# Optimization experiments

Hardware: AMD Instinct MI355X
Metric: run time of the kernel (lower is better)

The kernel has to match this reference:

```python
import jax, jax.numpy as jnp
import numpy as np

N, T, C = 8, 2048, 1024   # batch, seq_len, n_embd (== num_cls)
NUM_CLS = 1024
LID, TL = 6, 12


def setup_inputs() -> dict:
    key = jax.random.key(0)
    ks = jax.random.split(key, 5)
    s = 1.0 / np.sqrt(C)
    x = jax.random.normal(ks[0], (N, T, C), jnp.float32)
    Wk = jax.random.normal(ks[1], (C, C), jnp.float32) * s
    Wv = jax.random.normal(ks[2], (C, C), jnp.float32) * s
    Wr = jax.random.normal(ks[3], (C, C), jnp.float32) * s
    Wo = jax.random.normal(ks[4], (NUM_CLS, C), jnp.float32) * s
    # faithful time-parameter initialization from __init__
    r0 = LID / (TL - 1)            # ratio_0_to_1
    r1 = 1.0 - LID / TL            # ratio_1_to_almost0
    ddd = (np.arange(C, dtype=np.float32) / C).reshape(1, 1, C)
    time_mix_k = jnp.asarray(ddd ** r1)
    time_mix_v = jnp.asarray(ddd ** r1 + 0.3 * r0)
    time_mix_r = jnp.asarray(ddd ** (0.5 * r1))
    time_decay = jnp.zeros((C,), jnp.float32)                 # decay_speed init
    time_first = jnp.full((C,), np.log(0.3), jnp.float32)
    last_x = jnp.zeros((N, 1, C), jnp.float32)                # init_x repeated
    state = jnp.zeros((N, 3, 1, C), jnp.float32)              # init_state repeated
    return {"x": x, "it": 0, "Wk": Wk, "Wv": Wv, "Wr": Wr, "Wo": Wo,
            "time_mix_k": time_mix_k, "time_mix_v": time_mix_v,
            "time_mix_r": time_mix_r, "time_decay": time_decay,
            "time_first": time_first, "last_x": last_x, "state": state}


def _wkv_with_eps(w, u, k, v, state):
    """Numerically-stabilized RWKV wkv scan. k,v: (N,T,C); state: (N,3,1,C)."""
    alpha = state[:, 0, -1]  # (N,C)
    beta = state[:, 1, -1]
    eps = state[:, 2, -1]

    def step(carry, kv):
        a, b, e = carry
        kt, vt = kv                      # each (N,C)
        ukt = u + kt
        tau = jnp.maximum(ukt, e)
        e1 = jnp.exp(e - tau)
        e2 = jnp.exp(ukt - tau)
        wkv_t = (e1 * a + e2 * vt) / (e1 * b + e2)
        w_eps = e - w
        e_n = jnp.maximum(w_eps, kt)
        e1n = jnp.exp(w_eps - e_n)
        e2n = jnp.exp(kt - e_n)
        return (e1n * a + e2n * vt, e1n * b + e2n, e_n), wkv_t

    kT = jnp.swapaxes(k, 0, 1)  # (T,N,C)
    vT = jnp.swapaxes(v, 0, 1)
    (alpha, beta, eps), wkv = jax.lax.scan(step, (alpha, beta, eps), (kT, vT))
    wkv = jnp.swapaxes(wkv, 0, 1)  # (N,T,C)
    last_state = jnp.stack([alpha, beta, eps], axis=1)[:, :, None, :]  # (N,3,1,C)
    return wkv, last_state


def reference(x, it, Wk, Wv, Wr, Wo, time_mix_k, time_mix_v, time_mix_r,
              time_decay, time_first, last_x, state):
    # time-mix blend (last_x = init_x zeros, broadcast over T as in the source)
    k = (x * time_mix_k + last_x * (1.0 - time_mix_k)) @ Wk.T
    v = (x * time_mix_v + last_x * (1.0 - time_mix_v)) @ Wv.T
    r = (x * time_mix_r + last_x * (1.0 - time_mix_r)) @ Wr.T
    sr = jax.nn.sigmoid(r)
    w = jnp.exp(time_decay)
    u = time_first
    wkv, _last_state = _wkv_with_eps(w, u, k, v, state)
    rwkv = (wkv * sr) @ Wo.T  # (N,T,NUM_CLS)
    return rwkv
```

## Files before the change

### kernel.cpp

```cpp
#include <hip/hip_runtime.h>
#include <hip/hip_bf16.h>
#include <stdint.h>


typedef float f4 __attribute__((ext_vector_type(4)));
typedef short bh8 __attribute__((ext_vector_type(8)));
typedef unsigned int u32;
typedef unsigned short u16;

__device__ __forceinline__ u32 cvt2bf(float a, float b) {
    __hip_bfloat162 h = __float22bfloat162_rn(make_float2(a, b));
    u32 u; __builtin_memcpy(&u, &h, 4); return u;
}
__device__ __forceinline__ float b2f(u16 u) {
    u32 x = (u32)u << 16; float f; __builtin_memcpy(&f, &x, 4); return f;
}
__device__ __forceinline__ u16 f2b(float f) {
    __hip_bfloat16 h = __float2bfloat16(f);
    u16 u; __builtin_memcpy(&u, &h, 2); return u;
}
__device__ __forceinline__ void gld_lds16(const void* g, void* l) {
    __builtin_amdgcn_global_load_lds(
        (const __attribute__((address_space(1))) u32*)g,
        (__attribute__((address_space(3))) u32*)l, 16, 0, 0);
}


#define BAR() __builtin_amdgcn_s_barrier()

#define PH_MFMA(I0, J0) \
  BAR(); \
  asm volatile("s_waitcnt lgkmcnt(0)" ::: "memory"); \
  __builtin_amdgcn_s_setprio(1); \
  _Pragma("unroll") for (int ks = 0; ks < 2; ks++) \
  _Pragma("unroll") for (int i = 0; i < 4; i++) \
  _Pragma("unroll") for (int j = 0; j < 2; j++) \
    acc[(I0)+i][(J0)+j] = __builtin_amdgcn_mfma_f32_16x16x32_bf16( \
        af[i][ks], bf[(J0)+j][ks], acc[(I0)+i][(J0)+j], 0, 0, 0); \
  __builtin_amdgcn_s_setprio(0);

#define GBODY(cA, cB, nA, nB, KKN, STG) do { \
  const u16* ap0 = (cA) + (wm + fr) * 64 + cs0; \
  const u16* ap1 = (cA) + (wm + fr) * 64 + (cs0 ^ 32); \
  const u16* bp0 = (cB) + (wn + fr) * 64 + cs0; \
  const u16* bp1 = (cB) + (wn + fr) * 64 + (cs0 ^ 32); \
  bh8 af[4][2], bf[4][2]; \
   \
  _Pragma("unroll") for (int i = 0; i < 4; i++) { \
    af[i][0] = *(const bh8*)(ap0 + i * 1024); af[i][1] = *(const bh8*)(ap1 + i * 1024); } \
  _Pragma("unroll") for (int j = 0; j < 2; j++) { \
    bf[j][0] = *(const bh8*)(bp0 + j * 1024); bf[j][1] = *(const bh8*)(bp1 + j * 1024); } \
  if (STG) { \
    gld_lds16(gB + srcB_lane + (KKN),                 (nB) + w * 1024); \
    gld_lds16(gB + srcB_lane + 8192 + (KKN),          (nB) + w * 1024 + 512); \
    gld_lds16(gB + srcB_lane + 131072 + (KKN),        (nB) + 8192 + w * 1024); \
    gld_lds16(gB + srcB_lane + 131072 + 8192 + (KKN), (nB) + 8192 + w * 1024 + 512); } \
  PH_MFMA(0, 0); \
  BAR(); \
   \
  _Pragma("unroll") for (int j = 0; j < 2; j++) { \
    bf[2 + j][0] = *(const bh8*)(bp0 + (2 + j) * 1024); bf[2 + j][1] = *(const bh8*)(bp1 + (2 + j) * 1024); } \
  if (STG) { \
    gld_lds16(gA + srcA_lane + (KKN),          (nA) + w * 512); \
    gld_lds16(gA + srcA_lane + 131072 + (KKN), (nA) + 8192 + w * 512); } \
  PH_MFMA(0, 2); \
  if (STG) { asm volatile("s_waitcnt vmcnt(6)" ::: "memory"); } \
  else     { asm volatile("s_waitcnt vmcnt(0)" ::: "memory"); } \
  BAR(); \
   \
  _Pragma("unroll") for (int i = 0; i < 4; i++) { \
    af[i][0] = *(const bh8*)(ap0 + (4 + i) * 1024); af[i][1] = *(const bh8*)(ap1 + (4 + i) * 1024); } \
  if (STG) gld_lds16(gA + srcA_lane + 65536 + (KKN), (nA) + 4096 + w * 512); \
  PH_MFMA(4, 0); \
  BAR(); \
   \
  if (STG) gld_lds16(gA + srcA_lane + 131072 + 65536 + (KKN), (nA) + 12288 + w * 512); \
  PH_MFMA(4, 2); \
  if (STG) { asm volatile("s_waitcnt vmcnt(2)" ::: "memory"); } \
  BAR(); \
} while (0)

template<int EPI>
__global__ __launch_bounds__(512, 2) void gemm256(
    const u16* __restrict__ Ag, const u16* __restrict__ Bg, const float* __restrict__ bias,
    u16* __restrict__ Kb, u16* __restrict__ Vb, u16* __restrict__ SRb, float* __restrict__ Yf)
{
    __shared__ __align__(16) char pool[131072];
    u16* A0s = (u16*)pool;
    u16* B0s = A0s + 16384;
    u16* A1s = B0s + 16384;
    u16* B1s = A1s + 16384;

    const int bid = blockIdx.x;
    const int xcd = bid & 7;
    const int s   = bid >> 3;
    int p, mt, nt;
    if (EPI == 0) { p = s >> 5; int r = s & 31; nt = r & 3; mt = xcd * 8 + (r >> 2); }
    else          { p = 0;                      nt = s & 3; mt = xcd * 8 + (s >> 2); }
    const int n0 = nt * 256;
    const int m0 = mt * 256;

    const u16* gA = Ag + (size_t)m0 * 1024;
    const u16* gB = Bg + (EPI == 0 ? (size_t)p * 1048576 : 0) + (size_t)n0 * 1024;

    const int tid  = threadIdx.x;
    const int w    = tid >> 6;
    const int lane = tid & 63;
    const int wr = w >> 2, wc = w & 3;
    const int wm = wr * 128, wn = wc * 64;
    const int fr = lane & 15, quad = lane >> 4;
    const int cs0 = (quad ^ (fr & 7)) * 8;

    const int l8 = lane >> 3, l7 = lane & 7;
    const int chs = (l7 ^ l8) * 8;
    const int srcA_lane = (w * 8 + l8) * 1024 + chs;
    const int srcB_lane = (w * 16 + l8) * 1024 + chs;

    f4 acc[8][4];
#pragma unroll
    for (int i = 0; i < 8; i++)
#pragma unroll
        for (int j = 0; j < 4; j++) { f4 z = {0.f, 0.f, 0.f, 0.f}; acc[i][j] = z; }

#pragma unroll
    for (int q = 0; q < 4; q++)
        gld_lds16(gA + srcA_lane + q * 65536, A0s + q * 4096 + w * 512);
#pragma unroll
    for (int H = 0; H < 2; H++)
#pragma unroll
        for (int c = 0; c < 2; c++)
            gld_lds16(gB + srcB_lane + H * 131072 + c * 8192, B0s + H * 8192 + w * 1024 + c * 512);
    asm volatile("s_waitcnt vmcnt(0)" ::: "memory");
    BAR();

    for (int t = 0; t < 14; t += 2) {
        GBODY(A0s, B0s, A1s, B1s, (t + 1) * 64, true);
        GBODY(A1s, B1s, A0s, B0s, (t + 2) * 64, true);
    }
    GBODY(A0s, B0s, A1s, B1s, 15 * 64, true);
    GBODY(A1s, B1s, A0s, B0s, 0, false);

    if constexpr (EPI == 0) {
        const int batch = m0 >> 11;
        float bv[4];
#pragma unroll
        for (int j = 0; j < 4; j++) bv[j] = bias[p * 8192 + batch * 1024 + n0 + wn + j * 16 + fr];
        __syncthreads();
        u16* S = (u16*)pool;
#pragma unroll
        for (int i = 0; i < 8; i++)
#pragma unroll
            for (int j = 0; j < 4; j++)
#pragma unroll
                for (int r = 0; r < 4; r++) {
                    float v = acc[i][j][r] + bv[j];
                    if (p == 2) v = __fdividef(1.0f, 1.0f + __expf(-v));
                    int row = wm + i * 16 + quad * 4 + r;
                    int col = wn + j * 16 + fr;
                    int phys = (col >> 3) ^ (quad << 3);
                    S[row * 256 + phys * 8 + (col & 7)] = f2b(v);
                }
        __syncthreads();
        u16* Y = p == 0 ? Kb : (p == 1 ? Vb : SRb);
#pragma unroll
        for (int rep = 0; rep < 16; rep++) {
            int cid = rep * 512 + tid;
            int row = cid >> 5, ch = cid & 31;
            int phys = ch ^ (((row >> 2) & 3) << 3);
            uint4 val = *(const uint4*)(S + row * 256 + phys * 8);
            *(uint4*)(Y + (size_t)(m0 + row) * 1024 + n0 + ch * 8) = val;
        }
    } else {
        float* Sf = (float*)pool;
#pragma unroll
        for (int h = 0; h < 2; h++) {
            __syncthreads();
            if (wr == h) {
#pragma unroll
                for (int i = 0; i < 8; i++)
#pragma unroll
                    for (int j = 0; j < 4; j++)
#pragma unroll
                        for (int r = 0; r < 4; r++) {
                            int row = i * 16 + quad * 4 + r;
                            int col = wn + j * 16 + fr;
                            int phys = (col >> 2) ^ (quad << 4);
                            Sf[row * 256 + phys * 4 + (col & 3)] = acc[i][j][r];
                        }
            }
            __syncthreads();
#pragma unroll
            for (int rep = 0; rep < 16; rep++) {
                int cid = rep * 512 + tid;
                int row = cid >> 6, ch = cid & 63;
                int phys = ch ^ (((row >> 2) & 3) << 4);
                f4 val = *(const f4*)(Sf + row * 256 + phys * 4);
                *(f4*)(Yf + (size_t)(m0 + h * 128 + row) * 1024 + n0 + ch * 4) = val;
            }
        }
    }
}

__global__ __launch_bounds__(256) void prep_all(
    const float* __restrict__ x, const float* __restrict__ lastx,
    const float* __restrict__ Wk, const float* __restrict__ Wv,
    const float* __restrict__ Wr, const float* __restrict__ Wo,
    const float* __restrict__ tmk, const float* __restrict__ tmv, const float* __restrict__ tmr,
    u16* __restrict__ xb, u16* __restrict__ Wall, float* __restrict__ bias)
{
    int b = blockIdx.x;
    if (b < 16384) {
        int e = (b * 256 + threadIdx.x) << 2;
        f4 v = *(const f4*)(x + e);
        *(uint2*)(xb + e) = make_uint2(cvt2bf(v.x, v.y), cvt2bf(v.z, v.w));
    } else if (b < 20480) {
        int e = ((b - 16384) * 256 + threadIdx.x) << 2;
        int wid = e >> 20;
        int off = e & 1048575;
        int c = e & 1023;
        const float* src = wid == 0 ? Wk : (wid == 1 ? Wv : (wid == 2 ? Wr : Wo));
        f4 v = *(const f4*)(src + off);
        if (wid < 3) {
            const float* m = wid == 0 ? tmk : (wid == 1 ? tmv : tmr);
            v = v * *(const f4*)(m + c);
        }
        *(uint2*)(Wall + e) = make_uint2(cvt2bf(v.x, v.y), cvt2bf(v.z, v.w));
    } else {
        int wid = (b - 20480) * 4 + (threadIdx.x >> 6);
        int lane = threadIdx.x & 63;
        int proj = wid >> 10;
        int n = wid & 1023;
        const float* W = proj == 0 ? Wk : (proj == 1 ? Wv : Wr);
        const float* m = proj == 0 ? tmk : (proj == 1 ? tmv : tmr);
        float acc[8];
#pragma unroll
        for (int bb = 0; bb < 8; bb++) acc[bb] = 0.f;
        for (int c = lane; c < 1024; c += 64) {
            float wc = W[n * 1024 + c] * (1.0f - m[c]);
#pragma unroll
            for (int bb = 0; bb < 8; bb++) acc[bb] = fmaf(lastx[bb * 1024 + c], wc, acc[bb]);
        }
#pragma unroll
        for (int bb = 0; bb < 8; bb++) {
            float v = acc[bb];
#pragma unroll
            for (int sh = 32; sh >= 1; sh >>= 1) v += __shfl_xor(v, sh);
            if (lane == 0) bias[proj * 8192 + bb * 1024 + n] = v;
        }
    }
}

__global__ __launch_bounds__(256) void wkv_pass1(
    const u16* __restrict__ Kp, const u16* __restrict__ Vp,
    const float* __restrict__ tdec,
    float* __restrict__ Ca, float* __restrict__ Cb, float* __restrict__ Ce)
{
    int tid = blockIdx.x * 256 + threadIdx.x;
    int c = (tid & 511) << 1;
    int chunk = (tid >> 9) & 63;
    int n = tid >> 15;
    float w0 = __expf(tdec[c]), w1 = __expf(tdec[c + 1]);
    int base = (n * 2048 + chunk * 32) * 1024 + c;
    float a0 = 0.f, b0 = 0.f, e0 = -1e30f;
    float a1 = 0.f, b1 = 0.f, e1 = -1e30f;
#pragma unroll 4
    for (int i = 0; i < 32; i++) {
        u32 ku = *(const u32*)(Kp + base + (i << 10));
        u32 vu = *(const u32*)(Vp + base + (i << 10));
        float k0 = b2f((u16)ku), k1 = b2f((u16)(ku >> 16));
        float v0 = b2f((u16)vu), v1 = b2f((u16)(vu >> 16));
        float en0 = fmaxf(e0 - w0, k0);
        float f10 = __expf(e0 - w0 - en0), f20 = __expf(k0 - en0);
        a0 = fmaf(f10, a0, f20 * v0); b0 = fmaf(f10, b0, f20); e0 = en0;
        float en1 = fmaxf(e1 - w1, k1);
        float f11 = __expf(e1 - w1 - en1), f21 = __expf(k1 - en1);
        a1 = fmaf(f11, a1, f21 * v1); b1 = fmaf(f11, b1, f21); e1 = en1;
    }
    int oidx = ((n * 64 + chunk) << 10) + c;
    *(float2*)(Ca + oidx) = make_float2(a0, a1);
    *(float2*)(Cb + oidx) = make_float2(b0, b1);
    *(float2*)(Ce + oidx) = make_float2(e0, e1);
}

__global__ __launch_bounds__(256) void wkv_pass2(
    const float* __restrict__ state, const float* __restrict__ tdec,
    float* Ca, float* Cb, float* Ce)
{
    int tid = blockIdx.x * 256 + threadIdx.x;
    int c = tid & 1023;
    int n = tid >> 10;
    float a = state[(n * 3 + 0) * 1024 + c];
    float b = state[(n * 3 + 1) * 1024 + c];
    float e = state[(n * 3 + 2) * 1024 + c];
    float wL = __expf(tdec[c]) * 32.0f;
    for (int ch = 0; ch < 64; ++ch) {
        int idx = ((n * 64 + ch) << 10) + c;
        float ca = Ca[idx], cb = Cb[idx], ce = Ce[idx];
        Ca[idx] = a; Cb[idx] = b; Ce[idx] = e;
        float en = fmaxf(e - wL, ce);
        float f1 = __expf(e - wL - en);
        float f2 = __expf(ce - en);
        a = fmaf(f1, a, f2 * ca);
        b = fmaf(f1, b, f2 * cb);
        e = en;
    }
}

__global__ __launch_bounds__(256) void wkv_pass3(
    const u16* __restrict__ Kp, const u16* __restrict__ Vp, const u16* __restrict__ SRp,
    const float* __restrict__ Sa, const float* __restrict__ Sb, const float* __restrict__ Se,
    const float* __restrict__ tfirst, const float* __restrict__ tdec,
    u16* __restrict__ Pp)
{
    int tid = blockIdx.x * 256 + threadIdx.x;
    int c = (tid & 511) << 1;
    int chunk = (tid >> 9) & 63;
    int n = tid >> 15;
    int sidx = ((n * 64 + chunk) << 10) + c;
    float a0 = Sa[sidx], b0 = Sb[sidx], e0 = Se[sidx];
    float a1 = Sa[sidx + 1], b1 = Sb[sidx + 1], e1 = Se[sidx + 1];
    float u0 = tfirst[c], u1 = tfirst[c + 1];
    float w0 = __expf(tdec[c]), w1 = __expf(tdec[c + 1]);
    int base = (n * 2048 + chunk * 32) * 1024 + c;
#pragma unroll 2
    for (int i = 0; i < 32; i++) {
        u32 ku = *(const u32*)(Kp + base + (i << 10));
        u32 vu = *(const u32*)(Vp + base + (i << 10));
        u32 su = *(const u32*)(SRp + base + (i << 10));
        float k0 = b2f((u16)ku), k1 = b2f((u16)(ku >> 16));
        float v0 = b2f((u16)vu), v1 = b2f((u16)(vu >> 16));
        float s0 = b2f((u16)su), s1 = b2f((u16)(su >> 16));
        float t0 = fmaxf(u0 + k0, e0);
        float x10 = __expf(e0 - t0), x20 = __expf(u0 + k0 - t0);
        float wkv0 = __fdividef(fmaf(x10, a0, x20 * v0), fmaf(x10, b0, x20));
        float t1 = fmaxf(u1 + k1, e1);
        float x11 = __expf(e1 - t1), x21 = __expf(u1 + k1 - t1);
        float wkv1 = __fdividef(fmaf(x11, a1, x21 * v1), fmaf(x11, b1, x21));
        *(u32*)(Pp + base + (i << 10)) = (u32)f2b(wkv0 * s0) | ((u32)f2b(wkv1 * s1) << 16);
        float en0 = fmaxf(e0 - w0, k0);
        float f10 = __expf(e0 - w0 - en0), f20 = __expf(k0 - en0);
        a0 = fmaf(f10, a0, f20 * v0); b0 = fmaf(f10, b0, f20); e0 = en0;
        float en1 = fmaxf(e1 - w1, k1);
        float f11 = __expf(e1 - w1 - en1), f21 = __expf(k1 - en1);
        a1 = fmaf(f11, a1, f21 * v1); b1 = fmaf(f11, b1, f21); e1 = en1;
    }
}

extern "C" void kernel_launch(void* const* d_in, const int* in_sizes, int n_in,
                              void* d_out, int out_size, void* d_ws, size_t ws_size,
                              hipStream_t stream) {
    const float* x      = (const float*)d_in[0];
    const float* Wk     = (const float*)d_in[2];
    const float* Wv     = (const float*)d_in[3];
    const float* Wr     = (const float*)d_in[4];
    const float* Wo     = (const float*)d_in[5];
    const float* tmk    = (const float*)d_in[6];
    const float* tmv    = (const float*)d_in[7];
    const float* tmr    = (const float*)d_in[8];
    const float* tdec   = (const float*)d_in[9];
    const float* tfirst = (const float*)d_in[10];
    const float* lastx  = (const float*)d_in[11];
    const float* state  = (const float*)d_in[12];
    float* out = (float*)d_out;

    const size_t MB = 1024ull * 1024ull;
    char* ws = (char*)d_ws;
    u16* Kb   = (u16*)(ws);
    u16* Vb   = (u16*)(ws + 32 * MB);
    u16* SRb  = (u16*)(ws + 64 * MB);
    u16* xb   = (u16*)(ws + 96 * MB);
    u16* Wall = (u16*)(ws + 128 * MB);
    float* bias = (float*)(ws + 136 * MB);
    float* Ca = (float*)(ws + 137 * MB);
    float* Cb = (float*)(ws + 139 * MB);
    float* Ce = (float*)(ws + 141 * MB);
    u16* Pb = xb;

    dim3 blk(256);
    prep_all<<<21248, blk, 0, stream>>>(x, lastx, Wk, Wv, Wr, Wo, tmk, tmv, tmr, xb, Wall, bias);
    gemm256<0><<<dim3(768), dim3(512), 0, stream>>>(xb, Wall, bias, Kb, Vb, SRb, nullptr);
    wkv_pass1<<<1024, blk, 0, stream>>>(Kb, Vb, tdec, Ca, Cb, Ce);
    wkv_pass2<<<32, blk, 0, stream>>>(state, tdec, Ca, Cb, Ce);
    wkv_pass3<<<1024, blk, 0, stream>>>(Kb, Vb, SRb, Ca, Cb, Ce, tfirst, tdec, Pb);
    gemm256<1><<<dim3(256), dim3(512), 0, stream>>>(Pb, Wall + 3145728, nullptr,
                                                    nullptr, nullptr, nullptr, out);
}
```

Baseline: 358.7 us.

## Replace 256x256 GEMM with 256x128 tile, BK=32, triple-buffered LDS pipeline

Both GEMMs move from a 512-thread 256x256 tile with BK=64 double buffering to a 256-thread 256x128 tile with BK=32 and three LDS stages. The grid doubles and LDS drops from 128KB to 72KB, which should allow more blocks per CU and better load balance across the 256 CUs. Global loads are issued two stages ahead. The epilogues are rewritten to use padded LDS staging in place of XOR swizzles. The trade-off is lower arithmetic intensity per tile (more A reloads) and more barriers per unit of work.

```diff
diff --git a/kernel.cpp b/kernel.cpp
--- a/kernel.cpp
+++ b/kernel.cpp
@@ -25,79 +25,54 @@
         (__attribute__((address_space(3))) u32*)l, 16, 0, 0);
 }
 
-
 #define BAR() __builtin_amdgcn_s_barrier()
 
-#define PH_MFMA(I0, J0) \
+
+#define PH16(I0) \
   BAR(); \
   asm volatile("s_waitcnt lgkmcnt(0)" ::: "memory"); \
   __builtin_amdgcn_s_setprio(1); \
-  _Pragma("unroll") for (int ks = 0; ks < 2; ks++) \
   _Pragma("unroll") for (int i = 0; i < 4; i++) \
-  _Pragma("unroll") for (int j = 0; j < 2; j++) \
-    acc[(I0)+i][(J0)+j] = __builtin_amdgcn_mfma_f32_16x16x32_bf16( \
-        af[i][ks], bf[(J0)+j][ks], acc[(I0)+i][(J0)+j], 0, 0, 0); \
+  _Pragma("unroll") for (int j = 0; j < 4; j++) \
+    acc[(I0)+i][j] = __builtin_amdgcn_mfma_f32_16x16x32_bf16( \
+        af[i], bf[j], acc[(I0)+i][j], 0, 0, 0); \
   __builtin_amdgcn_s_setprio(0);
 
-#define GBODY(cA, cB, nA, nB, KKN, STG) do { \
-  const u16* ap0 = (cA) + (wm + fr) * 64 + cs0; \
-  const u16* ap1 = (cA) + (wm + fr) * 64 + (cs0 ^ 32); \
-  const u16* bp0 = (cB) + (wn + fr) * 64 + cs0; \
-  const u16* bp1 = (cB) + (wn + fr) * 64 + (cs0 ^ 32); \
-  bh8 af[4][2], bf[4][2]; \
-   \
-  _Pragma("unroll") for (int i = 0; i < 4; i++) { \
-    af[i][0] = *(const bh8*)(ap0 + i * 1024); af[i][1] = *(const bh8*)(ap1 + i * 1024); } \
-  _Pragma("unroll") for (int j = 0; j < 2; j++) { \
-    bf[j][0] = *(const bh8*)(bp0 + j * 1024); bf[j][1] = *(const bh8*)(bp1 + j * 1024); } \
+#define GB(CA, CB, NA, NB, KKN, STG, VM) do { \
+  bh8 af[4], bf[4]; \
+  _Pragma("unroll") for (int i = 0; i < 4; i++) af[i] = *(const bh8*)((CA) + apo + i * 512); \
+  _Pragma("unroll") for (int j = 0; j < 4; j++) bf[j] = *(const bh8*)((CB) + bpo + j * 512); \
   if (STG) { \
-    gld_lds16(gB + srcB_lane + (KKN),                 (nB) + w * 1024); \
-    gld_lds16(gB + srcB_lane + 8192 + (KKN),          (nB) + w * 1024 + 512); \
-    gld_lds16(gB + srcB_lane + 131072 + (KKN),        (nB) + 8192 + w * 1024); \
-    gld_lds16(gB + srcB_lane + 131072 + 8192 + (KKN), (nB) + 8192 + w * 1024 + 512); } \
-  PH_MFMA(0, 0); \
+    _Pragma("unroll") for (int q = 0; q < 4; q++) \
+      gld_lds16(gA + sAoff + q * 65536 + (KKN), (NA) + q * 2048 + w * 512); \
+    _Pragma("unroll") for (int h = 0; h < 2; h++) \
+      gld_lds16(gB + sAoff + h * 65536 + (KKN), (NB) + h * 2048 + w * 512); \
+  } \
+  PH16(0); \
   BAR(); \
-   \
-  _Pragma("unroll") for (int j = 0; j < 2; j++) { \
-    bf[2 + j][0] = *(const bh8*)(bp0 + (2 + j) * 1024); bf[2 + j][1] = *(const bh8*)(bp1 + (2 + j) * 1024); } \
-  if (STG) { \
-    gld_lds16(gA + srcA_lane + (KKN),          (nA) + w * 512); \
-    gld_lds16(gA + srcA_lane + 131072 + (KKN), (nA) + 8192 + w * 512); } \
-  PH_MFMA(0, 2); \
-  if (STG) { asm volatile("s_waitcnt vmcnt(6)" ::: "memory"); } \
-  else     { asm volatile("s_waitcnt vmcnt(0)" ::: "memory"); } \
-  BAR(); \
-   \
-  _Pragma("unroll") for (int i = 0; i < 4; i++) { \
-    af[i][0] = *(const bh8*)(ap0 + (4 + i) * 1024); af[i][1] = *(const bh8*)(ap1 + (4 + i) * 1024); } \
-  if (STG) gld_lds16(gA + srcA_lane + 65536 + (KKN), (nA) + 4096 + w * 512); \
-  PH_MFMA(4, 0); \
-  BAR(); \
-   \
-  if (STG) gld_lds16(gA + srcA_lane + 131072 + 65536 + (KKN), (nA) + 12288 + w * 512); \
-  PH_MFMA(4, 2); \
-  if (STG) { asm volatile("s_waitcnt vmcnt(2)" ::: "memory"); } \
+  _Pragma("unroll") for (int i = 0; i < 4; i++) af[i] = *(const bh8*)((CA) + apo + (4 + i) * 512); \
+  PH16(4); \
+  asm volatile("s_waitcnt vmcnt(" VM ")" ::: "memory"); \
   BAR(); \
 } while (0)
 
 template<int EPI>
-__global__ __launch_bounds__(512, 2) void gemm256(
+__global__ __launch_bounds__(256, 2) void gemm_ts(
     const u16* __restrict__ Ag, const u16* __restrict__ Bg, const float* __restrict__ bias,
     u16* __restrict__ Kb, u16* __restrict__ Vb, u16* __restrict__ SRb, float* __restrict__ Yf)
 {
-    __shared__ __align__(16) char pool[131072];
-    u16* A0s = (u16*)pool;
-    u16* B0s = A0s + 16384;
-    u16* A1s = B0s + 16384;
-    u16* B1s = A1s + 16384;
+    __shared__ __align__(16) char pool[73728];
+    u16* A0 = (u16*)pool;          u16* B0 = A0 + 8192;
+    u16* A1 = (u16*)(pool + 24576); u16* B1 = A1 + 8192;
+    u16* A2 = (u16*)(pool + 49152); u16* B2 = A2 + 8192;
 
     const int bid = blockIdx.x;
     const int xcd = bid & 7;
     const int s   = bid >> 3;
     int p, mt, nt;
-    if (EPI == 0) { p = s >> 5; int r = s & 31; nt = r & 3; mt = xcd * 8 + (r >> 2); }
-    else          { p = 0;                      nt = s & 3; mt = xcd * 8 + (s >> 2); }
-    const int n0 = nt * 256;
+    if (EPI == 0) { p = s >> 6; int r = s & 63; nt = r & 7; mt = xcd * 8 + (r >> 3); }
+    else          { p = 0;                      nt = s & 7; mt = xcd * 8 + (s >> 3); }
+    const int n0 = nt * 128;
     const int m0 = mt * 256;
 
     const u16* gA = Ag + (size_t)m0 * 1024;
@@ -106,15 +81,14 @@
     const int tid  = threadIdx.x;
     const int w    = tid >> 6;
     const int lane = tid & 63;
-    const int wr = w >> 2, wc = w & 3;
-    const int wm = wr * 128, wn = wc * 64;
+    const int wm = (w >> 1) * 128, wn = (w & 1) * 64;
     const int fr = lane & 15, quad = lane >> 4;
-    const int cs0 = (quad ^ (fr & 7)) * 8;
-
-    const int l8 = lane >> 3, l7 = lane & 7;
-    const int chs = (l7 ^ l8) * 8;
-    const int srcA_lane = (w * 8 + l8) * 1024 + chs;
-    const int srcB_lane = (w * 16 + l8) * 1024 + chs;
+    const int cs  = (quad ^ ((fr ^ (fr >> 2)) & 3)) * 8;
+    const int apo = (wm + fr) * 32 + cs;
+    const int bpo = (wn + fr) * 32 + cs;
+
+    const int sAoff = (w * 16 + (lane >> 2)) * 1024 +
+                      (((lane & 3) ^ ((lane >> 2) & 3) ^ ((lane >> 4) & 3))) * 8;
 
     f4 acc[8][4];
 #pragma unroll
@@ -123,81 +97,83 @@
         for (int j = 0; j < 4; j++) { f4 z = {0.f, 0.f, 0.f, 0.f}; acc[i][j] = z; }
 
 #pragma unroll
-    for (int q = 0; q < 4; q++)
-        gld_lds16(gA + srcA_lane + q * 65536, A0s + q * 4096 + w * 512);
-#pragma unroll
-    for (int H = 0; H < 2; H++)
-#pragma unroll
-        for (int c = 0; c < 2; c++)
-            gld_lds16(gB + srcB_lane + H * 131072 + c * 8192, B0s + H * 8192 + w * 1024 + c * 512);
-    asm volatile("s_waitcnt vmcnt(0)" ::: "memory");
+    for (int q = 0; q < 4; q++) gld_lds16(gA + sAoff + q * 65536, A0 + q * 2048 + w * 512);
+#pragma unroll
+    for (int h = 0; h < 2; h++) gld_lds16(gB + sAoff + h * 65536, B0 + h * 2048 + w * 512);
+#pragma unroll
+    for (int q = 0; q < 4; q++) gld_lds16(gA + sAoff + q * 65536 + 32, A1 + q * 2048 + w * 512);
+#pragma unroll
+    for (int h = 0; h < 2; h++) gld_lds16(gB + sAoff + h * 65536 + 32, B1 + h * 2048 + w * 512);
+    asm volatile("s_waitcnt vmcnt(6)" ::: "memory");
     BAR();
 
-    for (int t = 0; t < 14; t += 2) {
-        GBODY(A0s, B0s, A1s, B1s, (t + 1) * 64, true);
-        GBODY(A1s, B1s, A0s, B0s, (t + 2) * 64, true);
-    }
-    GBODY(A0s, B0s, A1s, B1s, 15 * 64, true);
-    GBODY(A1s, B1s, A0s, B0s, 0, false);
+    for (int t = 0; t < 30; t += 3) {
+        GB(A0, B0, A2, B2, (t + 2) * 32, 1, "6");
+        GB(A1, B1, A0, B0, (t + 3) * 32, 1, "6");
+        GB(A2, B2, A1, B1, (t + 4) * 32, 1, "6");
+    }
+    GB(A0, B0, A2, B2, 0, 0, "0");
+    GB(A1, B1, A2, B2, 0, 0, "0");
 
     if constexpr (EPI == 0) {
         const int batch = m0 >> 11;
         float bv[4];
 #pragma unroll
         for (int j = 0; j < 4; j++) bv[j] = bias[p * 8192 + batch * 1024 + n0 + wn + j * 16 + fr];
-        __syncthreads();
         u16* S = (u16*)pool;
-#pragma unroll
-        for (int i = 0; i < 8; i++)
-#pragma unroll
-            for (int j = 0; j < 4; j++)
-#pragma unroll
-                for (int r = 0; r < 4; r++) {
-                    float v = acc[i][j][r] + bv[j];
-                    if (p == 2) v = __fdividef(1.0f, 1.0f + __expf(-v));
-                    int row = wm + i * 16 + quad * 4 + r;
-                    int col = wn + j * 16 + fr;
-                    int phys = (col >> 3) ^ (quad << 3);
-                    S[row * 256 + phys * 8 + (col & 7)] = f2b(v);
-                }
-        __syncthreads();
         u16* Y = p == 0 ? Kb : (p == 1 ? Vb : SRb);
 #pragma unroll
-        for (int rep = 0; rep < 16; rep++) {
-            int cid = rep * 512 + tid;
-            int row = cid >> 5, ch = cid & 31;
-            int phys = ch ^ (((row >> 2) & 3) << 3);
-            uint4 val = *(const uint4*)(S + row * 256 + phys * 8);
-            *(uint4*)(Y + (size_t)(m0 + row) * 1024 + n0 + ch * 8) = val;
+        for (int h = 0; h < 2; h++) {
+            __syncthreads();
+            if ((w >> 1) == h) {
+#pragma unroll
+                for (int i = 0; i < 8; i++)
+#pragma unroll
+                    for (int j = 0; j < 4; j++)
+#pragma unroll
+                        for (int r = 0; r < 4; r++) {
+                            float v = acc[i][j][r] + bv[j];
+                            if (p == 2) v = __fdividef(1.0f, 1.0f + __expf(-v));
+                            int row = i * 16 + quad * 4 + r;
+                            int col = wn + j * 16 + fr;
+                            S[row * 136 + col] = f2b(v);
+                        }
+            }
+            __syncthreads();
+#pragma unroll
+            for (int rep = 0; rep < 8; rep++) {
+                int row = rep * 16 + (tid >> 4), ch = tid & 15;
+                uint4 val = *(const uint4*)(S + row * 136 + ch * 8);
+                *(uint4*)(Y + (size_t)(m0 + h * 128 + row) * 1024 + n0 + ch * 8) = val;
+            }
         }
     } else {
         float* Sf = (float*)pool;
 #pragma unroll
-        for (int h = 0; h < 2; h++) {
-            __syncthreads();
-            if (wr == h) {
-#pragma unroll
-                for (int i = 0; i < 8; i++)
-#pragma unroll
-                    for (int j = 0; j < 4; j++)
-#pragma unroll
-                        for (int r = 0; r < 4; r++) {
-                            int row = i * 16 + quad * 4 + r;
-                            int col = wn + j * 16 + fr;
-                            int phys = (col >> 2) ^ (quad << 4);
-                            Sf[row * 256 + phys * 4 + (col & 3)] = acc[i][j][r];
-                        }
+        for (int h = 0; h < 2; h++)
+#pragma unroll
+            for (int ih = 0; ih < 2; ih++) {
+                __syncthreads();
+                if ((w >> 1) == h) {
+#pragma unroll
+                    for (int ii = 0; ii < 4; ii++)
+#pragma unroll
+                        for (int j = 0; j < 4; j++)
+#pragma unroll
+                            for (int r = 0; r < 4; r++) {
+                                int row = ii * 16 + quad * 4 + r;
+                                int col = wn + j * 16 + fr;
+                                Sf[row * 132 + col] = acc[ih * 4 + ii][j][r];
+                            }
+                }
+                __syncthreads();
+#pragma unroll
+                for (int rep = 0; rep < 8; rep++) {
+                    int row = rep * 8 + (tid >> 5), ch = tid & 31;
+                    f4 val = *(const f4*)(Sf + row * 132 + ch * 4);
+                    *(f4*)(Yf + (size_t)(m0 + h * 128 + ih * 64 + row) * 1024 + n0 + ch * 4) = val;
+                }
             }
-            __syncthreads();
-#pragma unroll
-            for (int rep = 0; rep < 16; rep++) {
-                int cid = rep * 512 + tid;
-                int row = cid >> 6, ch = cid & 63;
-                int phys = ch ^ (((row >> 2) & 3) << 4);
-                f4 val = *(const f4*)(Sf + row * 256 + phys * 4);
-                *(f4*)(Yf + (size_t)(m0 + h * 128 + row) * 1024 + n0 + ch * 4) = val;
-            }
-        }
     }
 }
 
@@ -378,10 +354,10 @@
 
     dim3 blk(256);
     prep_all<<<21248, blk, 0, stream>>>(x, lastx, Wk, Wv, Wr, Wo, tmk, tmv, tmr, xb, Wall, bias);
-    gemm256<0><<<dim3(768), dim3(512), 0, stream>>>(xb, Wall, bias, Kb, Vb, SRb, nullptr);
+    gemm_ts<0><<<dim3(1536), blk, 0, stream>>>(xb, Wall, bias, Kb, Vb, SRb, nullptr);
     wkv_pass1<<<1024, blk, 0, stream>>>(Kb, Vb, tdec, Ca, Cb, Ce);
     wkv_pass2<<<32, blk, 0, stream>>>(state, tdec, Ca, Cb, Ce);
     wkv_pass3<<<1024, blk, 0, stream>>>(Kb, Vb, SRb, Ca, Cb, Ce, tfirst, tdec, Pb);
-    gemm256<1><<<dim3(256), dim3(512), 0, stream>>>(Pb, Wall + 3145728, nullptr,
-                                                    nullptr, nullptr, nullptr, out);
-}
+    gemm_ts<1><<<dim3(512), blk, 0, stream>>>(Pb, Wall + 3145728, nullptr,
+                                              nullptr, nullptr, nullptr, out);
+}
```

Result: slower. 378.5 us (+5.5%).

## Parallelize chunk-state carry with shuffle scan and widen wkv per-thread channels

Applied to the files above, without the earlier changes.

The chunk-carry pass now splits each channel's 64 chunks across 8 lanes. Each lane reduces its 8 chunks locally, the lanes combine their results with a log-step shuffle scan, and each lane then writes its prefix states. This replaces a 64-step serial loop running on only 32 blocks. Passes 1 and 3 now handle 4 channels per thread using 8-byte loads, which halves their grid size and gives fewer, wider memory transactions. The trade-off is extra exp work in the scan and less thread-level parallelism in passes 1 and 3.

```diff
diff --git a/kernel.cpp b/kernel.cpp
--- a/kernel.cpp
+++ b/kernel.cpp
@@ -256,53 +256,96 @@
     float* __restrict__ Ca, float* __restrict__ Cb, float* __restrict__ Ce)
 {
     int tid = blockIdx.x * 256 + threadIdx.x;
-    int c = (tid & 511) << 1;
-    int chunk = (tid >> 9) & 63;
-    int n = tid >> 15;
-    float w0 = __expf(tdec[c]), w1 = __expf(tdec[c + 1]);
+    int c = (tid & 255) << 2;
+    int chunk = (tid >> 8) & 63;
+    int n = tid >> 14;
+    float w[4], a[4], b[4], e[4];
+    f4 td = *(const f4*)(tdec + c);
+#pragma unroll
+    for (int j = 0; j < 4; j++) { w[j] = __expf(td[j]); a[j] = 0.f; b[j] = 0.f; e[j] = -1e30f; }
     int base = (n * 2048 + chunk * 32) * 1024 + c;
-    float a0 = 0.f, b0 = 0.f, e0 = -1e30f;
-    float a1 = 0.f, b1 = 0.f, e1 = -1e30f;
-#pragma unroll 4
+#pragma unroll 2
     for (int i = 0; i < 32; i++) {
-        u32 ku = *(const u32*)(Kp + base + (i << 10));
-        u32 vu = *(const u32*)(Vp + base + (i << 10));
-        float k0 = b2f((u16)ku), k1 = b2f((u16)(ku >> 16));
-        float v0 = b2f((u16)vu), v1 = b2f((u16)(vu >> 16));
-        float en0 = fmaxf(e0 - w0, k0);
-        float f10 = __expf(e0 - w0 - en0), f20 = __expf(k0 - en0);
-        a0 = fmaf(f10, a0, f20 * v0); b0 = fmaf(f10, b0, f20); e0 = en0;
-        float en1 = fmaxf(e1 - w1, k1);
-        float f11 = __expf(e1 - w1 - en1), f21 = __expf(k1 - en1);
-        a1 = fmaf(f11, a1, f21 * v1); b1 = fmaf(f11, b1, f21); e1 = en1;
+        uint2 ku = *(const uint2*)(Kp + base + (i << 10));
+        uint2 vu = *(const uint2*)(Vp + base + (i << 10));
+        float k[4] = { b2f((u16)ku.x), b2f((u16)(ku.x >> 16)), b2f((u16)ku.y), b2f((u16)(ku.y >> 16)) };
+        float v[4] = { b2f((u16)vu.x), b2f((u16)(vu.x >> 16)), b2f((u16)vu.y), b2f((u16)(vu.y >> 16)) };
+#pragma unroll
+        for (int j = 0; j < 4; j++) {
+            float en = fmaxf(e[j] - w[j], k[j]);
+            float f1 = __expf(e[j] - w[j] - en), f2 = __expf(k[j] - en);
+            a[j] = fmaf(f1, a[j], f2 * v[j]); b[j] = fmaf(f1, b[j], f2); e[j] = en;
+        }
     }
     int oidx = ((n * 64 + chunk) << 10) + c;
-    *(float2*)(Ca + oidx) = make_float2(a0, a1);
-    *(float2*)(Cb + oidx) = make_float2(b0, b1);
-    *(float2*)(Ce + oidx) = make_float2(e0, e1);
+    *(f4*)(Ca + oidx) = f4{a[0], a[1], a[2], a[3]};
+    *(f4*)(Cb + oidx) = f4{b[0], b[1], b[2], b[3]};
+    *(f4*)(Ce + oidx) = f4{e[0], e[1], e[2], e[3]};
 }
 
 __global__ __launch_bounds__(256) void wkv_pass2(
     const float* __restrict__ state, const float* __restrict__ tdec,
     float* Ca, float* Cb, float* Ce)
 {
-    int tid = blockIdx.x * 256 + threadIdx.x;
-    int c = tid & 1023;
-    int n = tid >> 10;
-    float a = state[(n * 3 + 0) * 1024 + c];
-    float b = state[(n * 3 + 1) * 1024 + c];
-    float e = state[(n * 3 + 2) * 1024 + c];
+    int t = blockIdx.x * 256 + threadIdx.x;
+    int g = t & 7;
+    int nc = t >> 3;
+    int c = nc & 1023;
+    int n = nc >> 10;
     float wL = __expf(tdec[c]) * 32.0f;
-    for (int ch = 0; ch < 64; ++ch) {
-        int idx = ((n * 64 + ch) << 10) + c;
-        float ca = Ca[idx], cb = Cb[idx], ce = Ce[idx];
-        Ca[idx] = a; Cb[idx] = b; Ce[idx] = e;
-        float en = fmaxf(e - wL, ce);
-        float f1 = __expf(e - wL - en);
-        float f2 = __expf(ce - en);
-        a = fmaf(f1, a, f2 * ca);
-        b = fmaf(f1, b, f2 * cb);
-        e = en;
+
+    float ca[8], cb[8], ce[8];
+    int base = ((n * 64 + g * 8) << 10) + c;
+#pragma unroll
+    for (int i = 0; i < 8; i++) {
+        ca[i] = Ca[base + (i << 10)];
+        cb[i] = Cb[base + (i << 10)];
+        ce[i] = Ce[base + (i << 10)];
+    }
+
+    float ga = 0.f, gb = 0.f, ge = -1e30f;
+#pragma unroll
+    for (int i = 0; i < 8; i++) {
+        float en = fmaxf(ge - wL, ce[i]);
+        float f1 = __expf(ge - wL - en), f2 = __expf(ce[i] - en);
+        ga = fmaf(f1, ga, f2 * ca[i]); gb = fmaf(f1, gb, f2 * cb[i]); ge = en;
+    }
+
+    float ia = ga, ib = gb, ie = ge, id = wL * 8.0f;
+#pragma unroll
+    for (int sdist = 1; sdist < 8; sdist <<= 1) {
+        float pa = __shfl_up(ia, sdist, 8);
+        float pb = __shfl_up(ib, sdist, 8);
+        float pe = __shfl_up(ie, sdist, 8);
+        float pd = __shfl_up(id, sdist, 8);
+        if (g >= sdist) {
+            float en = fmaxf(pe - id, ie);
+            float f1 = __expf(pe - id - en), f2 = __expf(ie - en);
+            ia = fmaf(f1, pa, f2 * ia); ib = fmaf(f1, pb, f2 * ib); ie = en;
+            id = pd + id;
+        }
+    }
+    float xa = __shfl_up(ia, 1, 8), xb = __shfl_up(ib, 1, 8);
+    float xe = __shfl_up(ie, 1, 8), xd = __shfl_up(id, 1, 8);
+
+    float a0 = state[(n * 3 + 0) * 1024 + c];
+    float b0 = state[(n * 3 + 1) * 1024 + c];
+    float e0 = state[(n * 3 + 2) * 1024 + c];
+    float sa, sb, se;
+    if (g == 0) { sa = a0; sb = b0; se = e0; }
+    else {
+        float en = fmaxf(e0 - xd, xe);
+        float f1 = __expf(e0 - xd - en), f2 = __expf(xe - en);
+        sa = fmaf(f1, a0, f2 * xa); sb = fmaf(f1, b0, f2 * xb); se = en;
+    }
+
+#pragma unroll
+    for (int i = 0; i < 8; i++) {
+        int idx = base + (i << 10);
+        Ca[idx] = sa; Cb[idx] = sb; Ce[idx] = se;
+        float en = fmaxf(se - wL, ce[i]);
+        float f1 = __expf(se - wL - en), f2 = __expf(ce[i] - en);
+        sa = fmaf(f1, sa, f2 * ca[i]); sb = fmaf(f1, sb, f2 * cb[i]); se = en;
     }
 }
 
@@ -313,36 +356,44 @@
     u16* __restrict__ Pp)
 {
     int tid = blockIdx.x * 256 + threadIdx.x;
-    int c = (tid & 511) << 1;
-    int chunk = (tid >> 9) & 63;
-    int n = tid >> 15;
+    int c = (tid & 255) << 2;
+    int chunk = (tid >> 8) & 63;
+    int n = tid >> 14;
     int sidx = ((n * 64 + chunk) << 10) + c;
-    float a0 = Sa[sidx], b0 = Sb[sidx], e0 = Se[sidx];
-    float a1 = Sa[sidx + 1], b1 = Sb[sidx + 1], e1 = Se[sidx + 1];
-    float u0 = tfirst[c], u1 = tfirst[c + 1];
-    float w0 = __expf(tdec[c]), w1 = __expf(tdec[c + 1]);
+    f4 av = *(const f4*)(Sa + sidx);
+    f4 bv = *(const f4*)(Sb + sidx);
+    f4 ev = *(const f4*)(Se + sidx);
+    f4 uv = *(const f4*)(tfirst + c);
+    f4 td = *(const f4*)(tdec + c);
+    float a[4], b[4], e[4], u[4], w[4];
+#pragma unroll
+    for (int j = 0; j < 4; j++) {
+        a[j] = av[j]; b[j] = bv[j]; e[j] = ev[j]; u[j] = uv[j]; w[j] = __expf(td[j]);
+    }
     int base = (n * 2048 + chunk * 32) * 1024 + c;
 #pragma unroll 2
     for (int i = 0; i < 32; i++) {
-        u32 ku = *(const u32*)(Kp + base + (i << 10));
-        u32 vu = *(const u32*)(Vp + base + (i << 10));
-        u32 su = *(const u32*)(SRp + base + (i << 10));
-        float k0 = b2f((u16)ku), k1 = b2f((u16)(ku >> 16));
-        float v0 = b2f((u16)vu), v1 = b2f((u16)(vu >> 16));
-        float s0 = b2f((u16)su), s1 = b2f((u16)(su >> 16));
-        float t0 = fmaxf(u0 + k0, e0);
-        float x10 = __expf(e0 - t0), x20 = __expf(u0 + k0 - t0);
-        float wkv0 = __fdividef(fmaf(x10, a0, x20 * v0), fmaf(x10, b0, x20));
-        float t1 = fmaxf(u1 + k1, e1);
-        float x11 = __expf(e1 - t1), x21 = __expf(u1 + k1 - t1);
-        float wkv1 = __fdividef(fmaf(x11, a1, x21 * v1), fmaf(x11, b1, x21));
-        *(u32*)(Pp + base + (i << 10)) = (u32)f2b(wkv0 * s0) | ((u32)f2b(wkv1 * s1) << 16);
-        float en0 = fmaxf(e0 - w0, k0);
-        float f10 = __expf(e0 - w0 - en0), f20 = __expf(k0 - en0);
-        a0 = fmaf(f10, a0, f20 * v0); b0 = fmaf(f10, b0, f20); e0 = en0;
-        float en1 = fmaxf(e1 - w1, k1);
-        float f11 = __expf(e1 - w1 - en1), f21 = __expf(k1 - en1);
-        a1 = fmaf(f11, a1, f21 * v1); b1 = fmaf(f11, b1, f21); e1 = en1;
+        uint2 ku = *(const uint2*)(Kp + base + (i << 10));
+        uint2 vu = *(const uint2*)(Vp + base + (i << 10));
+        uint2 su = *(const uint2*)(SRp + base + (i << 10));
+        float k[4] = { b2f((u16)ku.x), b2f((u16)(ku.x >> 16)), b2f((u16)ku.y), b2f((u16)(ku.y >> 16)) };
+        float v[4] = { b2f((u16)vu.x), b2f((u16)(vu.x >> 16)), b2f((u16)vu.y), b2f((u16)(vu.y >> 16)) };
+        float sg[4] = { b2f((u16)su.x), b2f((u16)(su.x >> 16)), b2f((u16)su.y), b2f((u16)(su.y >> 16)) };
+        u16 o[4];
+#pragma unroll
+        for (int j = 0; j < 4; j++) {
+            float tm = fmaxf(u[j] + k[j], e[j]);
+            float x1 = __expf(e[j] - tm), x2 = __expf(u[j] + k[j] - tm);
+            float wkv = __fdividef(fmaf(x1, a[j], x2 * v[j]), fmaf(x1, b[j], x2));
+            o[j] = f2b(wkv * sg[j]);
+            float en = fmaxf(e[j] - w[j], k[j]);
+            float f1 = __expf(e[j] - w[j] - en), f2 = __expf(k[j] - en);
+            a[j] = fmaf(f1, a[j], f2 * v[j]); b[j] = fmaf(f1, b[j], f2); e[j] = en;
+        }
+        uint2 ov;
+        ov.x = (u32)o[0] | ((u32)o[1] << 16);
+        ov.y = (u32)o[2] | ((u32)o[3] << 16);
+        *(uint2*)(Pp + base + (i << 10)) = ov;
     }
 }
 
@@ -379,9 +430,9 @@
     dim3 blk(256);
     prep_all<<<21248, blk, 0, stream>>>(x, lastx, Wk, Wv, Wr, Wo, tmk, tmv, tmr, xb, Wall, bias);
     gemm256<0><<<dim3(768), dim3(512), 0, stream>>>(xb, Wall, bias, Kb, Vb, SRb, nullptr);
-    wkv_pass1<<<1024, blk, 0, stream>>>(Kb, Vb, tdec, Ca, Cb, Ce);
-    wkv_pass2<<<32, blk, 0, stream>>>(state, tdec, Ca, Cb, Ce);
-    wkv_pass3<<<1024, blk, 0, stream>>>(Kb, Vb, SRb, Ca, Cb, Ce, tfirst, tdec, Pb);
+    wkv_pass1<<<512, blk, 0, stream>>>(Kb, Vb, tdec, Ca, Cb, Ce);
+    wkv_pass2<<<256, blk, 0, stream>>>(state, tdec, Ca, Cb, Ce);
+    wkv_pass3<<<512, blk, 0, stream>>>(Kb, Vb, SRb, Ca, Cb, Ce, tfirst, tdec, Pb);
     gemm256<1><<<dim3(256), dim3(512), 0, stream>>>(Pb, Wall + 3145728, nullptr,
                                                     nullptr, nullptr, nullptr, out);
 }
```

Result: faster. 345.1 us (-3.8%).
